# Optimization experiments

Hardware: AMD Instinct MI355X
Metric: run time of the kernel (lower is better)

Reference implementation:

```python
import jax, jax.numpy as jnp
import numpy as np

N_USERS = 52643
N_ITEMS = 91599
N = N_USERS + N_ITEMS  # 144242 nodes
M_PAIRS = 1_000_000    # user-item interactions -> 2M symmetric directed edges
D = 64


def setup_inputs() -> dict:
    key = jax.random.key(0)
    k1, k2, k3, k4, k5 = jax.random.split(key, 5)
    # bipartite interactions, symmetrized: A = [[0, R], [R^T, 0]]
    u = jax.random.randint(k1, (M_PAIRS,), 0, N_USERS, dtype=jnp.int32)
    it = jax.random.randint(k2, (M_PAIRS,), N_USERS, N, dtype=jnp.int32)
    row = jnp.concatenate([u, it])
    col = jnp.concatenate([it, u])
    embed = jax.random.normal(k3, (N, D), dtype=jnp.float32)
    W1 = jax.random.normal(k4, (D, D), dtype=jnp.float32) * 0.01  # linear.weight
    W2 = jax.random.normal(k5, (D, D), dtype=jnp.float32) * 0.01  # interActTransform.weight
    b1 = jnp.zeros((D,), jnp.float32)
    b2 = jnp.zeros((D,), jnp.float32)
    return {"embed": embed, "row": row, "col": col,
            "W1": W1, "b1": b1, "W2": W2, "b2": b2}


def reference(embed, row, col, W1, b1, W2, b2):
    n = embed.shape[0]
    # degree of symmetric A (row sums), D^-1/2 normalization
    deg = jax.ops.segment_sum(jnp.ones(row.shape, embed.dtype), row, num_segments=n)
    dinv = jnp.where(deg > 0, jax.lax.rsqrt(jnp.maximum(deg, 1.0)), 0.0)
    vals = dinv[row] * dinv[col]  # L = D^-1/2 A D^-1/2 (COO values)

    def spmm(x):  # [n, d] -> L @ x
        return jax.ops.segment_sum(vals[:, None] * x[col], row, num_segments=n)

    h1 = embed + spmm(embed)        # L1 @ embed, L1 = L + I
    h2 = spmm(embed * embed)        # L2 @ embed^2
    # nn.Linear: x @ W^T + b
    return (h1 @ W1.T + b1) + (h2 @ W2.T + b2)
```

## Files before the change

kernel.cpp:

```cpp
#include <hip/hip_runtime.h>


#define NB 256
#define MAXBUCK 608
#define RECCAP 8192
#define ZSCALE 64.0f
#define ZINV (1.0f / 64.0f)

typedef short bf16x8 __attribute__((ext_vector_type(8)));
typedef float f32x4 __attribute__((ext_vector_type(4)));

__device__ __forceinline__ float bflo(unsigned int u) {
    union { unsigned int i; float f; } c; c.i = u << 16; return c.f;
}
__device__ __forceinline__ float bfhi(unsigned int u) {
    union { unsigned int i; float f; } c; c.i = u & 0xffff0000u; return c.f;
}
__device__ __forceinline__ unsigned int f2bf(float f) {
    union { float f; unsigned int i; } c; c.f = f;
    unsigned int r = c.i + 0x7FFFu + ((c.i >> 16) & 1u);
    return r >> 16;
}
__device__ __forceinline__ unsigned int pk2(float a, float b) {
    return f2bf(a) | (f2bf(b) << 16);
}


__global__ __launch_bounds__(256) void k1_count(const int* __restrict__ row,
                                                const int* __restrict__ col,
                                                int* __restrict__ H,
                                                int* __restrict__ galloc,
                                                int Eh, int nbuck) {
    __shared__ int hist[MAXBUCK];
    int tid = threadIdx.x, b = blockIdx.x;
    if (b == 0 && tid == 0) *galloc = 0;
    for (int i = tid; i < nbuck; i += 256) hist[i] = 0;
    __syncthreads();
    int chunk = (((Eh + NB - 1) / NB) + 3) & ~3;
    int e0 = b * chunk;
    int len = Eh - e0;
    if (len > chunk) len = chunk;
    if (len < 0) len = 0;
    int len4 = len & ~3;
    for (int o = tid * 4; o < len4; o += 1024) {
        int4 u = *(const int4*)&row[e0 + o];
        int4 v = *(const int4*)&col[e0 + o];
        atomicAdd(&hist[u.x >> 8], 1); atomicAdd(&hist[v.x >> 8], 1);
        atomicAdd(&hist[u.y >> 8], 1); atomicAdd(&hist[v.y >> 8], 1);
        atomicAdd(&hist[u.z >> 8], 1); atomicAdd(&hist[v.z >> 8], 1);
        atomicAdd(&hist[u.w >> 8], 1); atomicAdd(&hist[v.w >> 8], 1);
    }
    if (tid < len - len4) {
        int e = e0 + len4 + tid;
        atomicAdd(&hist[row[e] >> 8], 1);
        atomicAdd(&hist[col[e] >> 8], 1);
    }
    __syncthreads();
    for (int i = tid; i < nbuck; i += 256) H[b * nbuck + i] = hist[i];
}

__global__ __launch_bounds__(256) void k2_colscan(const int* __restrict__ H,
                                                  int* __restrict__ Off,
                                                  int* __restrict__ btot,
                                                  int* __restrict__ bbase,
                                                  int* __restrict__ galloc,
                                                  const float4* __restrict__ W1_4,
                                                  const float4* __restrict__ W2_4,
                                                  int4* __restrict__ wfrag, int nbuck) {
    __shared__ int lds[256];
    int t = threadIdx.x, beta = blockIdx.x;
    int v = H[t * nbuck + beta];
    lds[t] = v;
    __syncthreads();
    for (int off = 1; off < 256; off <<= 1) {
        int x = (t >= off) ? lds[t - off] : 0;
        __syncthreads();
        lds[t] += x;
        __syncthreads();
    }
    Off[beta * NB + t] = lds[t] - v;
    if (t == 255) {
        int tot = lds[255];
        btot[beta] = tot;
        bbase[beta] = atomicAdd(galloc, tot);
    }
    if (beta < 4) {
        int idx = beta * 256 + t;
        int m = idx >> 9, tt = (idx >> 7) & 3, kf = (idx >> 6) & 1;
        int lane = idx & 63, L = lane & 15, hi = lane >> 4;
        int rowd = 16 * tt + L;
        const float4* Wp = (m ? W2_4 : W1_4) + (size_t)rowd * 16 + kf * 8 + hi * 2;
        float4 w0 = Wp[0], w1 = Wp[1];
        wfrag[idx] = make_int4(pk2(w0.x, w0.y), pk2(w0.z, w0.w),
                               pk2(w1.x, w1.y), pk2(w1.z, w1.w));
    }
}

__global__ __launch_bounds__(256) void k3_scatter(const int* __restrict__ row,
                                                  const int* __restrict__ col,
                                                  const int* __restrict__ Off,
                                                  const int* __restrict__ bbase,
                                                  unsigned int* __restrict__ rec,
                                                  int Eh, int nbuck) {
    __shared__ int cur[MAXBUCK];
    int tid = threadIdx.x, b = blockIdx.x;
    for (int i = tid; i < nbuck; i += 256) cur[i] = bbase[i] + Off[i * NB + b];
    __syncthreads();
    int chunk = (((Eh + NB - 1) / NB) + 3) & ~3;
    int e0 = b * chunk;
    int len = Eh - e0;
    if (len > chunk) len = chunk;
    if (len < 0) len = 0;
    int len4 = len & ~3;
    for (int o = tid * 4; o < len4; o += 1024) {
        int4 u = *(const int4*)&row[e0 + o];
        int4 v = *(const int4*)&col[e0 + o];
        int p;
        p = atomicAdd(&cur[u.x >> 8], 1); rec[p] = ((unsigned int)v.x << 8) | (u.x & 255);
        p = atomicAdd(&cur[v.x >> 8], 1); rec[p] = ((unsigned int)u.x << 8) | (v.x & 255);
        p = atomicAdd(&cur[u.y >> 8], 1); rec[p] = ((unsigned int)v.y << 8) | (u.y & 255);
        p = atomicAdd(&cur[v.y >> 8], 1); rec[p] = ((unsigned int)u.y << 8) | (v.y & 255);
        p = atomicAdd(&cur[u.z >> 8], 1); rec[p] = ((unsigned int)v.z << 8) | (u.z & 255);
        p = atomicAdd(&cur[v.z >> 8], 1); rec[p] = ((unsigned int)u.z << 8) | (v.z & 255);
        p = atomicAdd(&cur[u.w >> 8], 1); rec[p] = ((unsigned int)v.w << 8) | (u.w & 255);
        p = atomicAdd(&cur[v.w >> 8], 1); rec[p] = ((unsigned int)u.w << 8) | (v.w & 255);
    }
    if (tid < len - len4) {
        int e = e0 + len4 + tid;
        int u = row[e], v = col[e];
        int p = atomicAdd(&cur[u >> 8], 1);
        rec[p] = ((unsigned int)v << 8) | (u & 255);
        int q = atomicAdd(&cur[v >> 8], 1);
        rec[q] = ((unsigned int)u << 8) | (v & 255);
    }
}

__global__ __launch_bounds__(256) void k4_local(const unsigned int* __restrict__ rec,
                                                const int* __restrict__ bbase,
                                                const int* __restrict__ btot,
                                                int* __restrict__ start,
                                                int* __restrict__ send,
                                                float* __restrict__ dinv,
                                                int* __restrict__ scol, int n) {
    __shared__ int hist[256], lcur[256], lds[256];
    __shared__ unsigned int cache[RECCAP];
    int t = threadIdx.x, beta = blockIdx.x;
    int base = bbase[beta];
    int cnt = btot[beta];
    bool cached = cnt <= RECCAP;
    hist[t] = 0;
    __syncthreads();
    for (int r = t; r < cnt; r += 256) {
        unsigned int rr = rec[base + r];
        if (cached) cache[r] = rr;
        atomicAdd(&hist[rr & 255], 1);
    }
    __syncthreads();
    int h = hist[t];
    lds[t] = h;
    __syncthreads();
    for (int off = 1; off < 256; off <<= 1) {
        int x = (t >= off) ? lds[t - off] : 0;
        __syncthreads();
        lds[t] += x;
        __syncthreads();
    }
    int excl = lds[t] - h;
    int node = (beta << 8) + t;
    if (node < n) {
        start[node] = base + excl;
        send[node] = base + excl + h;
        dinv[node] = h > 0 ? rsqrtf((float)h) : 0.0f;
    }
    lcur[t] = base + excl;
    __syncthreads();
    for (int r = t; r < cnt; r += 256) {
        unsigned int rr = cached ? cache[r] : rec[base + r];
        int p = atomicAdd(&lcur[rr & 255], 1);
        scol[p] = (int)(rr >> 8);
    }
}

__global__ __launch_bounds__(256) void k_xform(
    const float4* __restrict__ embed4, const float* __restrict__ dinv,
    const int4* __restrict__ wfrag,
    const float* __restrict__ b1, const float* __restrict__ b2,
    unsigned int* __restrict__ y1p, unsigned int* __restrict__ zp8, int n) {
    int tid = threadIdx.x;
    int wave = tid >> 6, lane = tid & 63;
    int L = lane & 15, hi = lane >> 4;

    bf16x8 bfr[2][4][2];
#pragma unroll
    for (int m = 0; m < 2; m++)
#pragma unroll
        for (int t = 0; t < 4; t++)
#pragma unroll
            for (int kf = 0; kf < 2; kf++) {
                int4 raw = wfrag[((((m * 4 + t) * 2) + kf) << 6) + lane];
                bfr[m][t][kf] = *(bf16x8*)&raw;
            }

    int tb16 = blockIdx.x * 64 + wave * 16;
    int nodeA = tb16 + L;
    int nc = nodeA < n ? nodeA : n - 1;
    const float4* rowp = embed4 + (size_t)nc * 16;
    float4 a0 = rowp[hi * 2];
    float4 a1 = rowp[hi * 2 + 1];
    float4 a2 = rowp[8 + hi * 2];
    float4 a3 = rowp[8 + hi * 2 + 1];

    int4 e0 = make_int4(pk2(a0.x, a0.y), pk2(a0.z, a0.w), pk2(a1.x, a1.y), pk2(a1.z, a1.w));
    int4 e1 = make_int4(pk2(a2.x, a2.y), pk2(a2.z, a2.w), pk2(a3.x, a3.y), pk2(a3.z, a3.w));
    int4 q0 = make_int4(pk2(a0.x * a0.x, a0.y * a0.y), pk2(a0.z * a0.z, a0.w * a0.w),
                        pk2(a1.x * a1.x, a1.y * a1.y), pk2(a1.z * a1.z, a1.w * a1.w));
    int4 q1 = make_int4(pk2(a2.x * a2.x, a2.y * a2.y), pk2(a2.z * a2.z, a2.w * a2.w),
                        pk2(a3.x * a3.x, a3.y * a3.y), pk2(a3.z * a3.z, a3.w * a3.w));
    bf16x8 aE[2] = {*(bf16x8*)&e0, *(bf16x8*)&e1};
    bf16x8 aQ[2] = {*(bf16x8*)&q0, *(bf16x8*)&q1};

    f32x4 accY[4], accS[4];
#pragma unroll
    for (int t = 0; t < 4; t++) { accY[t] = (f32x4)0.f; accS[t] = (f32x4)0.f; }
#pragma unroll
    for (int kf = 0; kf < 2; kf++)
#pragma unroll
        for (int t = 0; t < 4; t++) {
            accY[t] = __builtin_amdgcn_mfma_f32_16x16x32_bf16(aE[kf], bfr[0][t][kf], accY[t], 0, 0, 0);
            accS[t] = __builtin_amdgcn_mfma_f32_16x16x32_bf16(aQ[kf], bfr[1][t][kf], accS[t], 0, 0, 0);
        }

    float bs0 = b1[L] + b2[L];
    float bs1 = b1[16 + L] + b2[16 + L];
    float bs2 = b1[32 + L] + b2[32 + L];
    float bs3 = b1[48 + L] + b2[48 + L];
#pragma unroll
    for (int r = 0; r < 4; r++) {
        int node = tb16 + 4 * hi + r;
        if (node >= n) continue;
        float di = dinv[node];
        float y0 = accY[0][r], y1 = accY[1][r], y2 = accY[2][r], y3 = accY[3][r];
        float s0 = accS[0][r], s1 = accS[1][r], s2 = accS[2][r], s3 = accS[3][r];
        size_t b32 = (size_t)node * 32;
        y1p[b32 + L]      = pk2(y0 + bs0, y1 + bs1);
        y1p[b32 + 16 + L] = pk2(y2 + bs2, y3 + bs3);
        float z0 = di * (y0 + s0) * ZSCALE;
        float z1 = di * (y1 + s1) * ZSCALE;
        float z2 = di * (y2 + s2) * ZSCALE;
        float z3 = di * (y3 + s3) * ZSCALE;
        int w = __builtin_amdgcn_cvt_pk_fp8_f32(z0, z1, 0, false);
        w = __builtin_amdgcn_cvt_pk_fp8_f32(z2, z3, w, true);
        zp8[(size_t)node * 16 + L] = (unsigned int)w;
    }
}

__global__ __launch_bounds__(256, 8) void k_main(
    const unsigned int* __restrict__ zp8, const unsigned int* __restrict__ y1p,
    const int* __restrict__ start, const int* __restrict__ send,
    const int* __restrict__ scol, const float* __restrict__ dinv,
    float* __restrict__ outf, int n) {
    int tid = threadIdx.x;
    int wave = tid >> 6, lane = tid & 63, g = lane >> 4, l = lane & 15;
    int i = blockIdx.x * 16 + wave * 4 + g;
    bool valid = i < n;
    int ii = valid ? i : 0;
    int s0 = start[ii];
    int s1 = valid ? send[ii] : s0;

    float4 acc = make_float4(0.f, 0.f, 0.f, 0.f);
    for (int e = s0; e < s1; e += 16) {
        int cnt = s1 - e;
        cnt = cnt > 16 ? 16 : cnt;
        int jv = scol[e + (l < cnt ? l : 0)];
#pragma unroll 8
        for (int k = 0; k < 16; k++) {
            int j = __shfl(jv, (g << 4) + k, 64);
            float m = (k < cnt) ? 1.0f : 0.0f;
            unsigned int w = zp8[(size_t)j * 16 + l];
            acc.x = fmaf(__builtin_amdgcn_cvt_f32_fp8(w, 0), m, acc.x);
            acc.y = fmaf(__builtin_amdgcn_cvt_f32_fp8(w, 1), m, acc.y);
            acc.z = fmaf(__builtin_amdgcn_cvt_f32_fp8(w, 2), m, acc.z);
            acc.w = fmaf(__builtin_amdgcn_cvt_f32_fp8(w, 3), m, acc.w);
        }
    }
    if (valid) {
        float ds = dinv[i] * ZINV;
        unsigned int ya = y1p[(size_t)i * 32 + l];
        unsigned int yb = y1p[(size_t)i * 32 + 16 + l];
        size_t base = (size_t)i * 64;
        outf[base + l]      = fmaf(ds, acc.x, bflo(ya));
        outf[base + 16 + l] = fmaf(ds, acc.y, bfhi(ya));
        outf[base + 32 + l] = fmaf(ds, acc.z, bflo(yb));
        outf[base + 48 + l] = fmaf(ds, acc.w, bfhi(yb));
    }
}

extern "C" void kernel_launch(void* const* d_in, const int* in_sizes, int n_in,
                              void* d_out, int out_size, void* d_ws, size_t ws_size,
                              hipStream_t stream) {
    const float* embed = (const float*)d_in[0];
    const int* row = (const int*)d_in[1];
    const int* col = (const int*)d_in[2];
    const float* W1 = (const float*)d_in[3];
    const float* b1 = (const float*)d_in[4];
    const float* W2 = (const float*)d_in[5];
    const float* b2 = (const float*)d_in[6];
    float* out = (float*)d_out;

    int n = in_sizes[0] / 64;
    int E = in_sizes[1];
    int Eh = E / 2;
    int nbuck = (n + 255) >> 8;
    size_t n64 = (size_t)n * 64;
    if (nbuck > MAXBUCK) return;
    if (n >= (1 << 18)) return;

    char* ws = (char*)d_ws;
    size_t off = 0;
    unsigned int* zp8 = (unsigned int*)(ws + off); off += n64;
    unsigned int* y1p = (unsigned int*)(ws + off); off += n64 * 2;
    unsigned int* rec = (unsigned int*)(ws + off); off += (size_t)E * 4;
    int* scol = (int*)(ws + off);                  off += (size_t)E * 4;
    int* H = (int*)(ws + off);                     off += (size_t)NB * nbuck * 4;
    int* Off = (int*)(ws + off);                   off += (size_t)nbuck * NB * 4;
    int* btot = (int*)(ws + off);                  off += (size_t)nbuck * 4;
    int* bbase = (int*)(ws + off);                 off += (size_t)nbuck * 4;
    int* start = (int*)(ws + off);                 off += (size_t)n * 4;
    int* send = (int*)(ws + off);                  off += (size_t)n * 4;
    float* dinv = (float*)(ws + off);              off += (size_t)n * 4;
    int4* wfrag = (int4*)(ws + off);               off += 1024 * 16;
    int* galloc = (int*)(ws + off);                off += 64;

    if (off > ws_size) return;

    k1_count<<<NB, 256, 0, stream>>>(row, col, H, galloc, Eh, nbuck);
    k2_colscan<<<nbuck, 256, 0, stream>>>(H, Off, btot, bbase, galloc,
                                          (const float4*)W1, (const float4*)W2,
                                          wfrag, nbuck);
    k3_scatter<<<NB, 256, 0, stream>>>(row, col, Off, bbase, rec, Eh, nbuck);
    k4_local<<<nbuck, 256, 0, stream>>>(rec, bbase, btot, start, send, dinv, scol, n);
    k_xform<<<(n + 63) / 64, 256, 0, stream>>>((const float4*)embed, dinv, wfrag,
                                               b1, b2, y1p, zp8, n);
    k_main<<<(n + 15) / 16, 256, 0, stream>>>(zp8, y1p, start, send, scol, dinv,
                                              out, n);
}
```

Baseline: 95.53 us.

## Fuse bucket-local CSR build with MFMA feature transform; pack start/end

The separate xform kernel is folded into the per-bucket local sort kernel. Each block now transforms its own 256 nodes in four rounds and reads degrees directly from the shared histogram instead of reloading dinv from global memory. Start and end offsets are stored as one int2 so k_main does a single load per node. This removes one kernel launch and a dependency round trip, but the xform work now runs on only about 564 blocks instead of about 2254, which cuts parallelism for that stage.

Result: faster. 88.79 us, median of 2 (-7.1%).

```diff
diff --git a/kernel.cpp b/kernel.cpp
--- a/kernel.cpp
+++ b/kernel.cpp
@@ -135,13 +135,13 @@
     }
 }
 
-__global__ __launch_bounds__(256) void k4_local(const unsigned int* __restrict__ rec,
-                                                const int* __restrict__ bbase,
-                                                const int* __restrict__ btot,
-                                                int* __restrict__ start,
-                                                int* __restrict__ send,
-                                                float* __restrict__ dinv,
-                                                int* __restrict__ scol, int n) {
+__global__ __launch_bounds__(256) void k4_fused(
+    const unsigned int* __restrict__ rec, const int* __restrict__ bbase,
+    const int* __restrict__ btot, int2* __restrict__ sse,
+    float* __restrict__ dinv, int* __restrict__ scol,
+    const float4* __restrict__ embed4, const int4* __restrict__ wfrag,
+    const float* __restrict__ b1, const float* __restrict__ b2,
+    unsigned int* __restrict__ y1p, unsigned int* __restrict__ zp8, int n) {
     __shared__ int hist[256], lcur[256], lds[256];
     __shared__ unsigned int cache[RECCAP];
     int t = threadIdx.x, beta = blockIdx.x;
@@ -166,11 +166,10 @@
         __syncthreads();
     }
     int excl = lds[t] - h;
-    int node = (beta << 8) + t;
-    if (node < n) {
-        start[node] = base + excl;
-        send[node] = base + excl + h;
-        dinv[node] = h > 0 ? rsqrtf((float)h) : 0.0f;
+    int node0 = (beta << 8) + t;
+    if (node0 < n) {
+        sse[node0] = make_int2(base + excl, base + excl + h);
+        dinv[node0] = h > 0 ? rsqrtf((float)h) : 0.0f;
     }
     lcur[t] = base + excl;
     __syncthreads();
@@ -179,93 +178,91 @@
         int p = atomicAdd(&lcur[rr & 255], 1);
         scol[p] = (int)(rr >> 8);
     }
-}
-
-__global__ __launch_bounds__(256) void k_xform(
-    const float4* __restrict__ embed4, const float* __restrict__ dinv,
-    const int4* __restrict__ wfrag,
-    const float* __restrict__ b1, const float* __restrict__ b2,
-    unsigned int* __restrict__ y1p, unsigned int* __restrict__ zp8, int n) {
-    int tid = threadIdx.x;
-    int wave = tid >> 6, lane = tid & 63;
+
+    int wave = t >> 6, lane = t & 63;
     int L = lane & 15, hi = lane >> 4;
 
     bf16x8 bfr[2][4][2];
 #pragma unroll
     for (int m = 0; m < 2; m++)
 #pragma unroll
-        for (int t = 0; t < 4; t++)
+        for (int tt = 0; tt < 4; tt++)
 #pragma unroll
             for (int kf = 0; kf < 2; kf++) {
-                int4 raw = wfrag[((((m * 4 + t) * 2) + kf) << 6) + lane];
-                bfr[m][t][kf] = *(bf16x8*)&raw;
+                int4 raw = wfrag[((((m * 4 + tt) * 2) + kf) << 6) + lane];
+                bfr[m][tt][kf] = *(bf16x8*)&raw;
             }
-
-    int tb16 = blockIdx.x * 64 + wave * 16;
-    int nodeA = tb16 + L;
-    int nc = nodeA < n ? nodeA : n - 1;
-    const float4* rowp = embed4 + (size_t)nc * 16;
-    float4 a0 = rowp[hi * 2];
-    float4 a1 = rowp[hi * 2 + 1];
-    float4 a2 = rowp[8 + hi * 2];
-    float4 a3 = rowp[8 + hi * 2 + 1];
-
-    int4 e0 = make_int4(pk2(a0.x, a0.y), pk2(a0.z, a0.w), pk2(a1.x, a1.y), pk2(a1.z, a1.w));
-    int4 e1 = make_int4(pk2(a2.x, a2.y), pk2(a2.z, a2.w), pk2(a3.x, a3.y), pk2(a3.z, a3.w));
-    int4 q0 = make_int4(pk2(a0.x * a0.x, a0.y * a0.y), pk2(a0.z * a0.z, a0.w * a0.w),
-                        pk2(a1.x * a1.x, a1.y * a1.y), pk2(a1.z * a1.z, a1.w * a1.w));
-    int4 q1 = make_int4(pk2(a2.x * a2.x, a2.y * a2.y), pk2(a2.z * a2.z, a2.w * a2.w),
-                        pk2(a3.x * a3.x, a3.y * a3.y), pk2(a3.z * a3.z, a3.w * a3.w));
-    bf16x8 aE[2] = {*(bf16x8*)&e0, *(bf16x8*)&e1};
-    bf16x8 aQ[2] = {*(bf16x8*)&q0, *(bf16x8*)&q1};
-
-    f32x4 accY[4], accS[4];
-#pragma unroll
-    for (int t = 0; t < 4; t++) { accY[t] = (f32x4)0.f; accS[t] = (f32x4)0.f; }
-#pragma unroll
-    for (int kf = 0; kf < 2; kf++)
-#pragma unroll
-        for (int t = 0; t < 4; t++) {
-            accY[t] = __builtin_amdgcn_mfma_f32_16x16x32_bf16(aE[kf], bfr[0][t][kf], accY[t], 0, 0, 0);
-            accS[t] = __builtin_amdgcn_mfma_f32_16x16x32_bf16(aQ[kf], bfr[1][t][kf], accS[t], 0, 0, 0);
-        }
 
     float bs0 = b1[L] + b2[L];
     float bs1 = b1[16 + L] + b2[16 + L];
     float bs2 = b1[32 + L] + b2[32 + L];
     float bs3 = b1[48 + L] + b2[48 + L];
-#pragma unroll
-    for (int r = 0; r < 4; r++) {
-        int node = tb16 + 4 * hi + r;
-        if (node >= n) continue;
-        float di = dinv[node];
-        float y0 = accY[0][r], y1 = accY[1][r], y2 = accY[2][r], y3 = accY[3][r];
-        float s0 = accS[0][r], s1 = accS[1][r], s2 = accS[2][r], s3 = accS[3][r];
-        size_t b32 = (size_t)node * 32;
-        y1p[b32 + L]      = pk2(y0 + bs0, y1 + bs1);
-        y1p[b32 + 16 + L] = pk2(y2 + bs2, y3 + bs3);
-        float z0 = di * (y0 + s0) * ZSCALE;
-        float z1 = di * (y1 + s1) * ZSCALE;
-        float z2 = di * (y2 + s2) * ZSCALE;
-        float z3 = di * (y3 + s3) * ZSCALE;
-        int w = __builtin_amdgcn_cvt_pk_fp8_f32(z0, z1, 0, false);
-        w = __builtin_amdgcn_cvt_pk_fp8_f32(z2, z3, w, true);
-        zp8[(size_t)node * 16 + L] = (unsigned int)w;
+
+    for (int rnd = 0; rnd < 4; rnd++) {
+        int loc16 = rnd * 64 + wave * 16;
+        int tb16 = (beta << 8) + loc16;
+        int nodeA = tb16 + L;
+        int nc = nodeA < n ? nodeA : n - 1;
+        const float4* rowp = embed4 + (size_t)nc * 16;
+        float4 a0 = rowp[hi * 2];
+        float4 a1 = rowp[hi * 2 + 1];
+        float4 a2 = rowp[8 + hi * 2];
+        float4 a3 = rowp[8 + hi * 2 + 1];
+
+        int4 e0 = make_int4(pk2(a0.x, a0.y), pk2(a0.z, a0.w), pk2(a1.x, a1.y), pk2(a1.z, a1.w));
+        int4 e1 = make_int4(pk2(a2.x, a2.y), pk2(a2.z, a2.w), pk2(a3.x, a3.y), pk2(a3.z, a3.w));
+        int4 q0 = make_int4(pk2(a0.x * a0.x, a0.y * a0.y), pk2(a0.z * a0.z, a0.w * a0.w),
+                            pk2(a1.x * a1.x, a1.y * a1.y), pk2(a1.z * a1.z, a1.w * a1.w));
+        int4 q1 = make_int4(pk2(a2.x * a2.x, a2.y * a2.y), pk2(a2.z * a2.z, a2.w * a2.w),
+                            pk2(a3.x * a3.x, a3.y * a3.y), pk2(a3.z * a3.z, a3.w * a3.w));
+        bf16x8 aE[2] = {*(bf16x8*)&e0, *(bf16x8*)&e1};
+        bf16x8 aQ[2] = {*(bf16x8*)&q0, *(bf16x8*)&q1};
+
+        f32x4 accY[4], accS[4];
+#pragma unroll
+        for (int tt = 0; tt < 4; tt++) { accY[tt] = (f32x4)0.f; accS[tt] = (f32x4)0.f; }
+#pragma unroll
+        for (int kf = 0; kf < 2; kf++)
+#pragma unroll
+            for (int tt = 0; tt < 4; tt++) {
+                accY[tt] = __builtin_amdgcn_mfma_f32_16x16x32_bf16(aE[kf], bfr[0][tt][kf], accY[tt], 0, 0, 0);
+                accS[tt] = __builtin_amdgcn_mfma_f32_16x16x32_bf16(aQ[kf], bfr[1][tt][kf], accS[tt], 0, 0, 0);
+            }
+
+#pragma unroll
+        for (int r = 0; r < 4; r++) {
+            int node = tb16 + 4 * hi + r;
+            if (node >= n) continue;
+            int hd = hist[loc16 + 4 * hi + r];
+            float di = hd > 0 ? rsqrtf((float)hd) : 0.0f;
+            float y0 = accY[0][r], y1 = accY[1][r], y2 = accY[2][r], y3 = accY[3][r];
+            float s0 = accS[0][r], s1 = accS[1][r], s2 = accS[2][r], s3 = accS[3][r];
+            size_t b32 = (size_t)node * 32;
+            y1p[b32 + L]      = pk2(y0 + bs0, y1 + bs1);
+            y1p[b32 + 16 + L] = pk2(y2 + bs2, y3 + bs3);
+            float z0 = di * (y0 + s0) * ZSCALE;
+            float z1 = di * (y1 + s1) * ZSCALE;
+            float z2 = di * (y2 + s2) * ZSCALE;
+            float z3 = di * (y3 + s3) * ZSCALE;
+            int w = __builtin_amdgcn_cvt_pk_fp8_f32(z0, z1, 0, false);
+            w = __builtin_amdgcn_cvt_pk_fp8_f32(z2, z3, w, true);
+            zp8[(size_t)node * 16 + L] = (unsigned int)w;
+        }
     }
 }
 
 __global__ __launch_bounds__(256, 8) void k_main(
     const unsigned int* __restrict__ zp8, const unsigned int* __restrict__ y1p,
-    const int* __restrict__ start, const int* __restrict__ send,
-    const int* __restrict__ scol, const float* __restrict__ dinv,
-    float* __restrict__ outf, int n) {
+    const int2* __restrict__ sse, const int* __restrict__ scol,
+    const float* __restrict__ dinv, float* __restrict__ outf, int n) {
     int tid = threadIdx.x;
     int wave = tid >> 6, lane = tid & 63, g = lane >> 4, l = lane & 15;
     int i = blockIdx.x * 16 + wave * 4 + g;
     bool valid = i < n;
     int ii = valid ? i : 0;
-    int s0 = start[ii];
-    int s1 = valid ? send[ii] : s0;
+    int2 se = sse[ii];
+    int s0 = se.x;
+    int s1 = valid ? se.y : se.x;
 
     float4 acc = make_float4(0.f, 0.f, 0.f, 0.f);
     for (int e = s0; e < s1; e += 16) {
@@ -325,8 +322,7 @@
     int* Off = (int*)(ws + off);                   off += (size_t)nbuck * NB * 4;
     int* btot = (int*)(ws + off);                  off += (size_t)nbuck * 4;
     int* bbase = (int*)(ws + off);                 off += (size_t)nbuck * 4;
-    int* start = (int*)(ws + off);                 off += (size_t)n * 4;
-    int* send = (int*)(ws + off);                  off += (size_t)n * 4;
+    int2* sse = (int2*)(ws + off);                 off += (size_t)n * 8;
     float* dinv = (float*)(ws + off);              off += (size_t)n * 4;
     int4* wfrag = (int4*)(ws + off);               off += 1024 * 16;
     int* galloc = (int*)(ws + off);                off += 64;
@@ -338,9 +334,8 @@
                                           (const float4*)W1, (const float4*)W2,
                                           wfrag, nbuck);
     k3_scatter<<<NB, 256, 0, stream>>>(row, col, Off, bbase, rec, Eh, nbuck);
-    k4_local<<<nbuck, 256, 0, stream>>>(rec, bbase, btot, start, send, dinv, scol, n);
-    k_xform<<<(n + 63) / 64, 256, 0, stream>>>((const float4*)embed, dinv, wfrag,
-                                               b1, b2, y1p, zp8, n);
-    k_main<<<(n + 15) / 16, 256, 0, stream>>>(zp8, y1p, start, send, scol, dinv,
-                                              out, n);
-}
+    k4_fused<<<nbuck, 256, 0, stream>>>(rec, bbase, btot, sse, dinv, scol,
+                                        (const float4*)embed, wfrag, b1, b2,
+                                        y1p, zp8, n);
+    k_main<<<(n + 15) / 16, 256, 0, stream>>>(zp8, y1p, sse, scol, dinv, out, n);
+}
```
